# Performance work log

Hardware: AMD Instinct MI355X
Metric: run time of the kernel (lower is better)

Reference implementation:

```python
import jax, jax.numpy as jnp
import numpy as np

# ---- static configuration (mirrors EarthSpecificBlock/EarthAttention3D) ----
WS = (2, 6, 12)                 # window_size (Z, H, W)
DIM = 192
HEADS = 6
DEPTH = 2
B, Z, H, W = 1, 8, 91, 180      # token grid entering the layer
PAD_H = (WS[1] - H % WS[1]) % WS[1]   # 5
PAD_W = (WS[2] - W % WS[2]) % WS[2]   # 0
HP, WP = H + PAD_H, W + PAD_W         # 96, 180
TOK = WS[0] * WS[1] * WS[2]           # 144 tokens per window
NZ, NH, NW = Z // WS[0], HP // WS[1], WP // WS[2]   # 4, 16, 15
TYPE_W = NZ * NH                      # 64 window types (Z x lat)
BIAS_ROWS = (2 * WS[2] - 1) * WS[1] * WS[1] * WS[0] * WS[0]  # 3312


def _construct_index():
    """Position index into the earth-specific bias table (EarthAttention3D._construct_index)."""
    zi = np.arange(WS[0]); zj = -np.arange(WS[0]) * WS[0]
    hi = np.arange(WS[1]); hj = -np.arange(WS[1]) * WS[1]
    w = np.arange(WS[2])
    c1 = np.stack(np.meshgrid(zi, hi, w, indexing='ij')).reshape(3, -1)
    c2 = np.stack(np.meshgrid(zj, hj, w, indexing='ij')).reshape(3, -1)
    coords = (c1[:, :, None] - c2[:, None, :]).transpose(1, 2, 0)
    coords[:, :, 2] += WS[2] - 1
    coords[:, :, 1] *= 2 * WS[2] - 1
    coords[:, :, 0] *= (2 * WS[2] - 1) * WS[1] * WS[1]
    return coords.sum(-1).reshape(-1)   # (TOK*TOK,)


def _gen_mask():
    """Shifted-window attention mask (gen_mask), shape (1, NW, TYPE_W, 1, TOK, TOK)."""
    m = np.zeros((1, Z, HP, WP, 1), np.float32)
    zs = (slice(0, -WS[0]), slice(-WS[0], -WS[0] // 2), slice(-WS[0] // 2, None))
    hs = (slice(0, -WS[1]), slice(-WS[1], -WS[1] // 2), slice(-WS[1] // 2, None))
    cnt = 0
    for zsl in zs:
        for hsl in hs:
            m[:, zsl, hsl, :, :] = cnt
            cnt += 1
    mw = m.reshape(1, NZ, WS[0], NH, WS[1], NW, WS[2], 1).transpose(0, 1, 3, 5, 2, 4, 6, 7)
    mw = mw.reshape(1, NZ, NH, NW, TOK)
    am = mw[:, :, :, :, None, :] - mw[:, :, :, :, :, None]
    am = np.where(am != 0, np.float32(-100.0), np.float32(0.0))
    return am.transpose(0, 3, 1, 2, 4, 5).reshape(1, NW, TYPE_W, 1, TOK, TOK)


POS_IDX = jnp.asarray(_construct_index())
MASK = jnp.asarray(_gen_mask())


def _ln(x, g, b):
    m = x.mean(-1, keepdims=True)
    v = ((x - m) ** 2).mean(-1, keepdims=True)
    return (x - m) * jax.lax.rsqrt(v + 1e-5) * g + b


def _block(x, qkv_w, qkv_b, proj_w, proj_b, bias_tab, g1, b1, g2, b2, w1, bm1, w2, bm2, roll):
    shortcut = x
    x = jnp.pad(x, ((0, 0), (0, 0), (0, PAD_H), (0, PAD_W), (0, 0)))
    if roll:
        x = jnp.roll(x, (-(WS[0] // 2), -(WS[1] // 2), -(WS[2] // 2)), axis=(1, 2, 3))
    # window partition: (B, NW, TYPE_W, TOK, C)
    xw = x.reshape(B, NZ, WS[0], NH, WS[1], NW, WS[2], DIM).transpose(0, 5, 1, 3, 2, 4, 6, 7)
    xw = xw.reshape(B, NW, TYPE_W, TOK, DIM)
    dh = DIM // HEADS
    qkv = (xw @ qkv_w + qkv_b).reshape(B, NW, TYPE_W, TOK, 3, HEADS, dh)
    qkv = qkv.transpose(4, 0, 1, 2, 5, 3, 6)   # (3, B, NW, TYPE_W, HEADS, TOK, dh)
    q, k, v = qkv[0], qkv[1], qkv[2]
    q = q * (dh ** -0.5)
    attn = jnp.einsum('bwphid,bwphjd->bwphij', q, k)
    bias = bias_tab[POS_IDX].reshape(TOK, TOK, TYPE_W, HEADS).transpose(2, 3, 0, 1)
    attn = attn + bias
    if roll:
        attn = attn + MASK
    attn = jax.nn.softmax(attn, axis=-1)
    out = jnp.einsum('bwphij,bwphjd->bwphid', attn, v)
    out = out.transpose(0, 1, 2, 4, 3, 5).reshape(B, NW, TYPE_W, TOK, DIM)
    out = out @ proj_w + proj_b
    # window merge back to (B, Z, HP, WP, C)
    x = out.reshape(B, NW, NZ, NH, WS[0], WS[1], WS[2], DIM).transpose(0, 2, 4, 3, 5, 1, 6, 7)
    x = x.reshape(B, Z, HP, WP, DIM)
    if roll:
        x = jnp.roll(x, (WS[0] // 2, WS[1] // 2, WS[2] // 2), axis=(1, 2, 3))
    x = x[:, :, :H, :W]
    x = shortcut + _ln(x, g1, b1)           # post-norm residual, as in source
    h = jax.nn.gelu(x @ w1 + bm1, approximate=False)
    h = h @ w2 + bm2
    return x + _ln(h, g2, b2)


def setup_inputs() -> dict:
    key = jax.random.key(0)
    ks = jax.random.split(key, 8)
    s = 0.02
    return {
        'x': jax.random.normal(ks[0], (B, Z, H, W, DIM), jnp.float32),
        'qkv_w': jax.random.normal(ks[1], (DEPTH, DIM, 3 * DIM), jnp.float32) * s,
        'qkv_b': jnp.zeros((DEPTH, 3 * DIM), jnp.float32),
        'proj_w': jax.random.normal(ks[2], (DEPTH, DIM, DIM), jnp.float32) * s,
        'proj_b': jnp.zeros((DEPTH, DIM), jnp.float32),
        'bias_tab': jax.random.normal(ks[3], (DEPTH, BIAS_ROWS, TYPE_W, HEADS), jnp.float32) * s,
        'norm1_g': jnp.ones((DEPTH, DIM), jnp.float32),
        'norm1_b': jnp.zeros((DEPTH, DIM), jnp.float32),
        'norm2_g': jnp.ones((DEPTH, DIM), jnp.float32),
        'norm2_b': jnp.zeros((DEPTH, DIM), jnp.float32),
        'mlp_w1': jax.random.normal(ks[4], (DEPTH, DIM, 4 * DIM), jnp.float32) * s,
        'mlp_b1': jnp.zeros((DEPTH, 4 * DIM), jnp.float32),
        'mlp_w2': jax.random.normal(ks[5], (DEPTH, 4 * DIM, DIM), jnp.float32) * s,
        'mlp_b2': jnp.zeros((DEPTH, DIM), jnp.float32),
    }


def reference(x, qkv_w, qkv_b, proj_w, proj_b, bias_tab, norm1_g, norm1_b,
              norm2_g, norm2_b, mlp_w1, mlp_b1, mlp_w2, mlp_b2):
    for i in range(DEPTH):
        x = _block(x, qkv_w[i], qkv_b[i], proj_w[i], proj_b[i], bias_tab[i],
                   norm1_g[i], norm1_b[i], norm2_g[i], norm2_b[i],
                   mlp_w1[i], mlp_b1[i], mlp_w2[i], mlp_b2[i], roll=(i % 2 == 1))
    return x
```

## Files before the change

### kernel.cpp

```cpp
#include <hip/hip_runtime.h>
#include <math.h>

#define NTOK   131040
#define NTOKW  138240

typedef __attribute__((ext_vector_type(8))) short bf16x8;
typedef __attribute__((ext_vector_type(8))) unsigned short u16x8;
typedef __attribute__((ext_vector_type(4))) float f32x4;
typedef __attribute__((ext_vector_type(2))) float f32x2;

__device__ __forceinline__ float b2f(unsigned short u){
  union { unsigned u; float f; } v; v.u = ((unsigned)u) << 16; return v.f;
}
__device__ __forceinline__ unsigned short f2b(float f){
  union { float f; unsigned u; } v; v.f = f;
  unsigned r = v.u + 0x7FFFu + ((v.u >> 16) & 1u);
  return (unsigned short)(r >> 16);
}
__device__ __forceinline__ float gelu_fast(float x){
  float t = 0.79788456080286536f * (x + 0.044715f * x * x * x);
  float e = __expf(2.0f * t);
  float th = 1.0f - 2.0f * __builtin_amdgcn_rcpf(e + 1.0f);
  return 0.5f * x * (1.0f + th);
}
__device__ __forceinline__ unsigned pk_bf16(float lo, float hi){
  unsigned r;
  asm("v_cvt_pk_bf16_f32 %0, %1, %2" : "=v"(r) : "v"(lo), "v"(hi));
  return r;
}
__device__ __forceinline__ void lds_barrier(){
  asm volatile("s_waitcnt lgkmcnt(0)" ::: "memory");
  __builtin_amdgcn_sched_barrier(0);
  __builtin_amdgcn_s_barrier();
  __builtin_amdgcn_sched_barrier(0);
}

__global__ __launch_bounds__(256) void transp(const float* __restrict__ src,
                                              unsigned short* __restrict__ dst,
                                              int K, int N){
  int i = blockIdx.x*256 + threadIdx.x;
  if (i < K*N){
    int n = i / K, k = i % K;
    dst[i] = f2b(src[(size_t)k*N + n]);
  }
}

__global__ __launch_bounds__(256) void bias_pre(
    const float* __restrict__ btab,
    unsigned short* __restrict__ bw,
    int roll)
{
  int gid = blockIdx.x*256 + threadIdx.x;
  int pair = gid / 20736;
  int rem  = gid % 20736;
  int i = rem / 144, j = rem % 144;
  int tw = pair / 6, head = pair % 6;
  int ia = i/72, ib = (i%72)/12, ic = i%12;
  int ja = j/72, jb = (j%72)/12, jc = j%12;
  int idx = (ia + 2*ja)*828 + (ib + 6*jb)*23 + (ic - jc + 11);
  float v = btab[(size_t)idx*384 + tw*6 + head];
  if (roll){
    int nz = tw >> 4, nh = tw & 15;
    int zi = nz*2+ia, hi = nh*6+ib, zj = nz*2+ja, hj = nh*6+jb;
    int ri = 3*((zi<6)?0:((zi<7)?1:2)) + ((hi<90)?0:((hi<93)?1:2));
    int rj = 3*((zj<6)?0:((zj<7)?1:2)) + ((hj<90)?0:((hj<93)?1:2));
    if (ri != rj) v -= 100.0f;
  }
  bw[gid] = f2b(v);
}

__global__ __launch_bounds__(256) void gather_win(const float* __restrict__ x,
                                                  unsigned short* __restrict__ xw,
                                                  int roll){
  int gid = blockIdx.x*256 + threadIdx.x;
  int row = gid / 24;
  int dp  = gid % 24;
  int tok = row % 144;
  int wt  = row / 144;
  int tw  = wt & 63;
  int w   = wt >> 6;
  int nz = tw >> 4, nh = tw & 15;
  int wz = tok / 72; int rem = tok % 72; int wh = rem / 12; int ww = rem % 12;
  int z = nz*2 + wz, h = nh*6 + wh, wc = w*12 + ww;
  if (roll){ z = (z+1)&7; h = (h+3)%96; wc = (wc+6)%180; }
  int d0 = dp*8;
  u16x8 o;
  if (h < 91){
    const float* s = x + ((size_t)((z*91 + h)*180 + wc))*192 + d0;
    #pragma unroll
    for (int i=0;i<8;i++) o[i] = f2b(s[i]);
  } else {
    #pragma unroll
    for (int i=0;i<8;i++) o[i] = 0;
  }
  *(u16x8*)(xw + (size_t)row*192 + d0) = o;
}

__global__ __launch_bounds__(512) void gemm_k192(
    const unsigned short* __restrict__ A,
    const unsigned short* __restrict__ Bt,
    const float* __restrict__ bias,
    unsigned short* __restrict__ C,
    int N)
{
  __shared__ unsigned short Bst[192][200];
  int m0 = blockIdx.x * 128;
  int n0 = blockIdx.y * 192;
  int t = threadIdx.x;
  int lane = t & 63, w = t >> 6;
  int wm = w >> 2, wn = w & 3;
  int lg = lane >> 4, lr = lane & 15;

  #pragma unroll
  for (int i=0;i<9;i++){
    int idx = t + i*512;
    int r = idx / 24, c = (idx % 24)*8;
    *(u16x8*)&Bst[r][c] = *(const u16x8*)(Bt + (size_t)(n0 + r)*192 + c);
  }
  __syncthreads();

  const unsigned short* aRow = A + (size_t)(m0 + wm*64 + lr)*192 + lg*8;

  f32x4 acc[4][3];
  #pragma unroll
  for (int a=0;a<4;a++)
    #pragma unroll
    for (int b=0;b<3;b++) acc[a][b] = (f32x4){0.f,0.f,0.f,0.f};

  bf16x8 aP[2][6];
  #pragma unroll
  for (int ks=0; ks<6; ks++) aP[0][ks] = *(const bf16x8*)(aRow + ks*32);

  #pragma unroll
  for (int rt=0; rt<4; rt++){
    if (rt < 3){
      const unsigned short* an = aRow + (size_t)(rt+1)*16*192;
      #pragma unroll
      for (int ks=0; ks<6; ks++) aP[(rt+1)&1][ks] = *(const bf16x8*)(an + ks*32);
    }
    #pragma unroll
    for (int ks=0; ks<6; ks++){
      bf16x8 b0 = *(const bf16x8*)&Bst[wn*48 +      lr][ks*32 + lg*8];
      bf16x8 b1 = *(const bf16x8*)&Bst[wn*48 + 16 + lr][ks*32 + lg*8];
      bf16x8 b2 = *(const bf16x8*)&Bst[wn*48 + 32 + lr][ks*32 + lg*8];
      bf16x8 af = aP[rt&1][ks];
      acc[rt][0] = __builtin_amdgcn_mfma_f32_16x16x32_bf16(af, b0, acc[rt][0], 0,0,0);
      acc[rt][1] = __builtin_amdgcn_mfma_f32_16x16x32_bf16(af, b1, acc[rt][1], 0,0,0);
      acc[rt][2] = __builtin_amdgcn_mfma_f32_16x16x32_bf16(af, b2, acc[rt][2], 0,0,0);
    }
  }

  #pragma unroll
  for (int rt=0; rt<4; rt++){
    #pragma unroll
    for (int fn=0; fn<3; fn++){
      int colg = n0 + wn*48 + fn*16 + lr;
      float bv = bias[colg];
      #pragma unroll
      for (int r=0;r<4;r++){
        int rowg = m0 + wm*64 + rt*16 + lg*4 + r;
        C[(size_t)rowg*N + colg] = f2b(acc[rt][fn][r] + bv);
      }
    }
  }
}

__global__ __launch_bounds__(576) void attn_win(
    const unsigned short* __restrict__ qkv,
    const unsigned short* __restrict__ bw,
    unsigned short* __restrict__ outp)
{
  __shared__ union {
    struct { unsigned short Qs[144][32]; unsigned short Ks[144][40]; } qk;
    unsigned short Ps[144][160];
  } U;
  __shared__ unsigned short Vst[32][160];

  int b = blockIdx.x;
  int head = b % 6;
  int wt = b / 6;
  int tw = wt & 63;
  int t = threadIdx.x;
  int lane = t & 63;
  int wv = t >> 6;
  int lg = lane >> 4, lr = lane & 15;

  {
    int tok = t >> 2, c0 = (t & 3)*8;
    size_t base = ((size_t)wt*144 + tok)*576 + head*32 + c0;
    u16x8 qv = *(const u16x8*)(qkv + base);
    u16x8 kv = *(const u16x8*)(qkv + base + 192);
    u16x8 vv = *(const u16x8*)(qkv + base + 384);
    u16x8 qs;
    #pragma unroll
    for (int i=0;i<8;i++) qs[i] = f2b(b2f(qv[i]) * 0.17677669529663687f);
    *(u16x8*)&U.qk.Qs[tok][c0] = qs;
    *(u16x8*)&U.qk.Ks[tok][c0] = kv;
    #pragma unroll
    for (int i=0;i<8;i++) Vst[c0+i][tok] = vv[i];
  }
  if (t < 512) Vst[t >> 4][144 + (t & 15)] = 0;
  __syncthreads();

  float s[9][4];
  {
    bf16x8 a = *(const bf16x8*)&U.qk.Qs[wv*16 + lr][lg*8];
    #pragma unroll
    for (int ct=0; ct<9; ct++){
      bf16x8 bb = *(const bf16x8*)&U.qk.Ks[ct*16 + lr][lg*8];
      f32x4 d = {0.f,0.f,0.f,0.f};
      d = __builtin_amdgcn_mfma_f32_16x16x32_bf16(a, bb, d, 0,0,0);
      s[ct][0]=d[0]; s[ct][1]=d[1]; s[ct][2]=d[2]; s[ct][3]=d[3];
    }
  }

  {
    const unsigned short* bp = bw + (size_t)(tw*6 + head)*20736;
    int i0 = wv*16 + lg*4;
    #pragma unroll
    for (int ct=0; ct<9; ct++){
      int j = ct*16 + lr;
      #pragma unroll
      for (int r=0;r<4;r++)
        s[ct][r] += b2f(bp[(i0 + r)*144 + j]);
    }
  }

  float mx[4] = {-1e30f,-1e30f,-1e30f,-1e30f};
  #pragma unroll
  for (int ct=0; ct<9; ct++)
    #pragma unroll
    for (int r=0;r<4;r++) mx[r] = fmaxf(mx[r], s[ct][r]);
  #pragma unroll
  for (int off=1; off<16; off<<=1)
    #pragma unroll
    for (int r=0;r<4;r++) mx[r] = fmaxf(mx[r], __shfl_xor(mx[r], off));
  float sm[4] = {0.f,0.f,0.f,0.f};
  #pragma unroll
  for (int ct=0; ct<9; ct++)
    #pragma unroll
    for (int r=0;r<4;r++){ s[ct][r] = __expf(s[ct][r] - mx[r]); sm[r] += s[ct][r]; }
  #pragma unroll
  for (int off=1; off<16; off<<=1)
    #pragma unroll
    for (int r=0;r<4;r++) sm[r] += __shfl_xor(sm[r], off);
  float inv[4];
  #pragma unroll
  for (int r=0;r<4;r++) inv[r] = 1.0f / sm[r];

  lds_barrier();

  #pragma unroll
  for (int ct=0; ct<9; ct++)
    #pragma unroll
    for (int r=0;r<4;r++)
      U.Ps[wv*16 + lg*4 + r][ct*16 + lr] = f2b(s[ct][r] * inv[r]);
  #pragma unroll
  for (int r=0;r<4;r++) U.Ps[wv*16 + lg*4 + r][144 + lr] = 0;
  __syncthreads();

  #pragma unroll
  for (int ct2=0; ct2<2; ct2++){
    f32x4 o = {0.f,0.f,0.f,0.f};
    #pragma unroll
    for (int kt=0; kt<5; kt++){
      bf16x8 a  = *(const bf16x8*)&U.Ps[wv*16 + lr][kt*32 + lg*8];
      bf16x8 bb = *(const bf16x8*)&Vst[ct2*16 + lr][kt*32 + lg*8];
      o = __builtin_amdgcn_mfma_f32_16x16x32_bf16(a, bb, o, 0,0,0);
    }
    size_t rb = ((size_t)wt*144 + wv*16 + lg*4)*192 + head*32 + ct2*16 + lr;
    #pragma unroll
    for (int r=0;r<4;r++) outp[rb + (size_t)r*192] = f2b(o[r]);
  }
}

__global__ __launch_bounds__(256) void unwin_ln(
  const unsigned short* __restrict__ ywin,
  const float* __restrict__ xsrc,
  const float* __restrict__ g, const float* __restrict__ bb,
  float* __restrict__ outf, unsigned short* __restrict__ outb, int roll)
{
  int tok = blockIdx.x*4 + (threadIdx.x>>6);
  if (tok >= NTOK) return;
  int lane = threadIdx.x & 63;
  int z = tok / (91*180);
  int rem = tok % (91*180);
  int h = rem / 180, wc = rem % 180;
  int zz=z, hh=h, ww=wc;
  if (roll){ zz = (z+7)&7; hh = (h+93)%96; ww = (wc+174)%180; }
  int nz = zz>>1, wz = zz&1;
  int nh = hh/6,  wh = hh%6;
  int nw = ww/12, w2 = ww%12;
  size_t row = ((size_t)(nw*64 + nz*16 + nh))*144 + wz*72 + wh*12 + w2;
  const unsigned short* yr = ywin + row*192;
  float v[3]; float s=0.f, ss=0.f;
  #pragma unroll
  for (int i=0;i<3;i++){ v[i] = b2f(yr[lane + i*64]); s += v[i]; ss += v[i]*v[i]; }
  #pragma unroll
  for (int off=32; off>=1; off>>=1){ s += __shfl_xor(s, off); ss += __shfl_xor(ss, off); }
  float mean = s * (1.0f/192.0f);
  float var = ss * (1.0f/192.0f) - mean*mean;
  float rinv = rsqrtf(var + 1e-5f);
  size_t tb = (size_t)tok*192;
  #pragma unroll
  for (int i=0;i<3;i++){
    int d = lane + i*64;
    float o = xsrc[tb + d] + ((v[i]-mean)*rinv*g[d] + bb[d]);
    outf[tb+d] = o;
    outb[tb+d] = f2b(o);
  }
}

__global__ __launch_bounds__(512) void mlp_fused_ln(
    const unsigned short* __restrict__ A,
    const unsigned short* __restrict__ W1t,
    const float* __restrict__ bias1,
    const unsigned short* __restrict__ W2t,
    const float* __restrict__ mbias2,
    const float* __restrict__ xmid,
    const float* __restrict__ lng,
    const float* __restrict__ lnb,
    float* __restrict__ outF,
    int M)
{
  __shared__ unsigned short W1s[32][196];
  __shared__ unsigned short W2s[192][44];
  __shared__ unsigned short Hs[8][32][40];
  __shared__ float b1s[768];
  __shared__ float eps[576];
  int m0 = blockIdx.x*256;
  int t = threadIdx.x, lane = t & 63, w = t >> 6;
  int lg = lane >> 4, lr = lane & 15;

  bf16x8 afrA[6], afrB[6];
  {
    int ra = m0 + w*32 + lr, rb = ra + 16;
    if (ra < M){
      const unsigned short* ap = A + (size_t)ra*192 + lg*8;
      #pragma unroll
      for (int ks=0; ks<6; ks++) afrA[ks] = *(const bf16x8*)(ap + ks*32);
    } else {
      #pragma unroll
      for (int ks=0; ks<6; ks++)
        #pragma unroll
        for (int j=0;j<8;j++) afrA[ks][j] = 0;
    }
    if (rb < M){
      const unsigned short* ap = A + (size_t)rb*192 + lg*8;
      #pragma unroll
      for (int ks=0; ks<6; ks++) afrB[ks] = *(const bf16x8*)(ap + ks*32);
    } else {
      #pragma unroll
      for (int ks=0; ks<6; ks++)
        #pragma unroll
        for (int j=0;j<8;j++) afrB[ks][j] = 0;
    }
  }

  b1s[t] = bias1[t];
  if (t < 256) b1s[512 + t] = bias1[512 + t];
  if (t < 192){ eps[t] = mbias2[t]; eps[192 + t] = lng[t]; eps[384 + t] = lnb[t]; }

  int i1r[2], i1c[2], i2r[2], i2c[2];
  #pragma unroll
  for (int i=0;i<2;i++){
    int idx = t + i*512;
    i1r[i] = idx/24; i1c[i] = (idx%24)*8;
    i2r[i] = idx/4;  i2c[i] = (idx&3)*8;
  }
  bool g2nd = (t + 512) < 768;

  u16x8 w1r[2], w2r[2];
  w1r[0] = *(const u16x8*)(W1t + (size_t)i1r[0]*192 + i1c[0]);
  w2r[0] = *(const u16x8*)(W2t + (size_t)i2r[0]*768 + i2c[0]);
  if (g2nd){
    w1r[1] = *(const u16x8*)(W1t + (size_t)i1r[1]*192 + i1c[1]);
    w2r[1] = *(const u16x8*)(W2t + (size_t)i2r[1]*768 + i2c[1]);
  }

  f32x4 accA[12], accB[12];
  #pragma unroll
  for (int i=0;i<12;i++){ accA[i] = (f32x4){0.f,0.f,0.f,0.f}; accB[i] = (f32x4){0.f,0.f,0.f,0.f}; }

  for (int it=0; it<24; ++it){
    int hc = it*32;
    *(u16x8*)&W1s[i1r[0]][i1c[0]] = w1r[0];
    *(u16x8*)&W2s[i2r[0]][i2c[0]] = w2r[0];
    if (g2nd){
      *(u16x8*)&W1s[i1r[1]][i1c[1]] = w1r[1];
      *(u16x8*)&W2s[i2r[1]][i2c[1]] = w2r[1];
    }
    if (it < 23){
      int hc2 = hc + 32;
      w1r[0] = *(const u16x8*)(W1t + (size_t)(hc2 + i1r[0])*192 + i1c[0]);
      w2r[0] = *(const u16x8*)(W2t + (size_t)i2r[0]*768 + hc2 + i2c[0]);
      if (g2nd){
        w1r[1] = *(const u16x8*)(W1t + (size_t)(hc2 + i1r[1])*192 + i1c[1]);
        w2r[1] = *(const u16x8*)(W2t + (size_t)i2r[1]*768 + hc2 + i2c[1]);
      }
    }
    lds_barrier();

    f32x4 h0a = (f32x4){0.f,0.f,0.f,0.f}, h1a = h0a, h0b = h0a, h1b = h0a;
    #pragma unroll
    for (int ks=0; ks<6; ks++){
      bf16x8 b0  = *(const bf16x8*)&W1s[2*lr    ][ks*32 + lg*8];
      bf16x8 b1f = *(const bf16x8*)&W1s[2*lr + 1][ks*32 + lg*8];
      h0a = __builtin_amdgcn_mfma_f32_16x16x32_bf16(afrA[ks], b0,  h0a, 0,0,0);
      h1a = __builtin_amdgcn_mfma_f32_16x16x32_bf16(afrA[ks], b1f, h1a, 0,0,0);
      h0b = __builtin_amdgcn_mfma_f32_16x16x32_bf16(afrB[ks], b0,  h0b, 0,0,0);
      h1b = __builtin_amdgcn_mfma_f32_16x16x32_bf16(afrB[ks], b1f, h1b, 0,0,0);
    }
    float bb0 = b1s[hc + 2*lr];
    float bb1 = b1s[hc + 2*lr + 1];
    #pragma unroll
    for (int r=0;r<4;r++){
      *(unsigned*)&Hs[w][lg*4 + r][2*lr] =
          pk_bf16(gelu_fast(h0a[r] + bb0), gelu_fast(h1a[r] + bb1));
      *(unsigned*)&Hs[w][16 + lg*4 + r][2*lr] =
          pk_bf16(gelu_fast(h0b[r] + bb0), gelu_fast(h1b[r] + bb1));
    }
    bf16x8 paA = *(const bf16x8*)&Hs[w][lr][lg*8];
    bf16x8 paB = *(const bf16x8*)&Hs[w][16 + lr][lg*8];
    #pragma unroll
    for (int f=0; f<6; f++){
      bf16x8 c0 = *(const bf16x8*)&W2s[f*32 + 2*lr    ][lg*8];
      bf16x8 c1 = *(const bf16x8*)&W2s[f*32 + 2*lr + 1][lg*8];
      accA[2*f]   = __builtin_amdgcn_mfma_f32_16x16x32_bf16(paA, c0, accA[2*f],   0,0,0);
      accA[2*f+1] = __builtin_amdgcn_mfma_f32_16x16x32_bf16(paA, c1, accA[2*f+1], 0,0,0);
      accB[2*f]   = __builtin_amdgcn_mfma_f32_16x16x32_bf16(paB, c0, accB[2*f],   0,0,0);
      accB[2*f+1] = __builtin_amdgcn_mfma_f32_16x16x32_bf16(paB, c1, accB[2*f+1], 0,0,0);
    }
    lds_barrier();
  }

  #pragma unroll
  for (int gsel=0; gsel<2; gsel++){
    f32x4* acc = gsel ? accB : accA;
    #pragma unroll
    for (int r=0;r<4;r++){
      int row = m0 + w*32 + gsel*16 + lg*4 + r;
      float s = 0.f, ss = 0.f;
      #pragma unroll
      for (int f=0; f<6; f++){
        float v0 = acc[2*f][r]   + eps[f*32 + 2*lr];
        float v1 = acc[2*f+1][r] + eps[f*32 + 2*lr + 1];
        s += v0 + v1; ss += v0*v0 + v1*v1;
      }
      #pragma unroll
      for (int off=1; off<16; off<<=1){ s += __shfl_xor(s, off); ss += __shfl_xor(ss, off); }
      float mean = s * (1.0f/192.0f);
      float var  = ss * (1.0f/192.0f) - mean*mean;
      float rinv = rsqrtf(var + 1e-5f);
      if (row < M){
        size_t base = (size_t)row*192;
        #pragma unroll
        for (int f=0; f<6; f++){
          int c0 = f*32 + 2*lr;
          float v0 = acc[2*f][r]   + eps[c0];
          float v1 = acc[2*f+1][r] + eps[c0 + 1];
          f32x2 xm = *(const f32x2*)&xmid[base + c0];
          f32x2 o;
          o[0] = xm[0] + (v0 - mean)*rinv*eps[192 + c0]     + eps[384 + c0];
          o[1] = xm[1] + (v1 - mean)*rinv*eps[192 + c0 + 1] + eps[384 + c0 + 1];
          *(f32x2*)&outF[base + c0] = o;
        }
      }
    }
  }
}

extern "C" void kernel_launch(void* const* d_in, const int* in_sizes, int n_in,
                              void* d_out, int out_size, void* d_ws, size_t ws_size,
                              hipStream_t stream)
{
  const float* x_in    = (const float*)d_in[0];
  const float* qkvw    = (const float*)d_in[1];
  const float* qkvbias = (const float*)d_in[2];
  const float* projw   = (const float*)d_in[3];
  const float* projbias= (const float*)d_in[4];
  const float* btab    = (const float*)d_in[5];
  const float* n1g = (const float*)d_in[6];
  const float* n1b = (const float*)d_in[7];
  const float* n2g = (const float*)d_in[8];
  const float* n2b = (const float*)d_in[9];
  const float* w1  = (const float*)d_in[10];
  const float* b1  = (const float*)d_in[11];
  const float* w2  = (const float*)d_in[12];
  const float* b2  = (const float*)d_in[13];
  float* outp = (float*)d_out;

  const size_t REG_A = (size_t)NTOKW*192;
  const size_t REG_B = (size_t)NTOKW*576;
  const size_t W_QT  = (size_t)2*576*192;
  const size_t W_PT  = (size_t)2*192*192;
  const size_t W_1T  = (size_t)2*768*192;
  const size_t W_2T  = (size_t)2*192*768;
  const size_t TOT_SH = REG_A + REG_B + W_QT + W_PT + W_1T + W_2T;
  const size_t NEEDED = TOT_SH*2 + (size_t)NTOK*192*4;
  if (ws_size < NEEDED) return;

  unsigned short* ws16 = (unsigned short*)d_ws;
  size_t off = 0;
  unsigned short* regA = ws16 + off; off += REG_A;
  unsigned short* regB = ws16 + off; off += REG_B;
  unsigned short* wqt  = ws16 + off; off += W_QT;
  unsigned short* wpt  = ws16 + off; off += W_PT;
  unsigned short* w1t  = ws16 + off; off += W_1T;
  unsigned short* w2t  = ws16 + off; off += W_2T;
  float* xmidf = (float*)(ws16 + off);
  unsigned short* bw = (unsigned short*)xmidf;

  for (int dep=0; dep<2; dep++){
    transp<<<(192*576+255)/256,256,0,stream>>>(qkvw + (size_t)dep*192*576,
                                               wqt + (size_t)dep*576*192, 192, 576);
    transp<<<(192*192+255)/256,256,0,stream>>>(projw + (size_t)dep*192*192,
                                               wpt + (size_t)dep*192*192, 192, 192);
    transp<<<(192*768+255)/256,256,0,stream>>>(w1 + (size_t)dep*192*768,
                                               w1t + (size_t)dep*768*192, 192, 768);
    transp<<<(768*192+255)/256,256,0,stream>>>(w2 + (size_t)dep*768*192,
                                               w2t + (size_t)dep*192*768, 768, 192);
  }

  for (int dep=0; dep<2; dep++){
    int roll = dep;
    const float* xs = (dep==0) ? x_in : outp;
    float* xout = outp;

    gather_win<<<NTOKW*24/256, 256, 0, stream>>>(xs, regA, roll);

    dim3 g1(NTOKW/128, 3);
    gemm_k192<<<g1, 512, 0, stream>>>(regA, wqt + (size_t)dep*576*192,
                                      qkvbias + dep*576, regB, 576);

    bias_pre<<<(64*6*20736)/256, 256, 0, stream>>>(btab + (size_t)dep*3312*384, bw, roll);

    attn_win<<<960*6, 576, 0, stream>>>(regB, bw, regA);

    dim3 g2(NTOKW/128, 1);
    gemm_k192<<<g2, 512, 0, stream>>>(regA, wpt + (size_t)dep*192*192,
                                      projbias + dep*192, regB, 192);

    unwin_ln<<<NTOK/4, 256, 0, stream>>>(regB, xs, n1g + dep*192, n1b + dep*192,
                                         xmidf, regA, roll);

    mlp_fused_ln<<<(NTOK+255)/256, 512, 0, stream>>>(
        regA, w1t + (size_t)dep*768*192, b1 + dep*768,
        w2t + (size_t)dep*192*768, b2 + dep*192,
        xmidf, n2g + dep*192, n2b + dep*192, xout, NTOK);
  }
}
```

Measured before the change: 1.083 ms.

## Pre-swizzle attention bias into MFMA fragment order and shrink MLP block size

The bias precompute kernel now writes the per-window bias in the exact register-fragment order used by the attention kernel, padded to five 8-wide vectors per lane. Attention threads can then load their bias with five 16-byte vector loads issued before the barrier, instead of 36 scattered scalar bf16 loads after the QK MFMA. Separately, the fused MLP kernel moves to 256 threads and 128 rows per block, doubling the grid and changing the W1 LDS padding, which shifts occupancy and the weight-staging work per block. The padded bias layout writes slightly more data.

```diff
diff --git a/kernel.cpp b/kernel.cpp
--- a/kernel.cpp
+++ b/kernel.cpp
@@ -51,22 +51,34 @@
     int roll)
 {
   int gid = blockIdx.x*256 + threadIdx.x;
-  int pair = gid / 20736;
-  int rem  = gid % 20736;
-  int i = rem / 144, j = rem % 144;
-  int tw = pair / 6, head = pair % 6;
-  int ia = i/72, ib = (i%72)/12, ic = i%12;
-  int ja = j/72, jb = (j%72)/12, jc = j%12;
-  int idx = (ia + 2*ja)*828 + (ib + 6*jb)*23 + (ic - jc + 11);
-  float v = btab[(size_t)idx*384 + tw*6 + head];
-  if (roll){
-    int nz = tw >> 4, nh = tw & 15;
-    int zi = nz*2+ia, hi = nh*6+ib, zj = nz*2+ja, hj = nh*6+jb;
-    int ri = 3*((zi<6)?0:((zi<7)?1:2)) + ((hi<90)?0:((hi<93)?1:2));
-    int rj = 3*((zj<6)?0:((zj<7)?1:2)) + ((hj<90)?0:((hj<93)?1:2));
-    if (ri != rj) v -= 100.0f;
-  }
-  bw[gid] = f2b(v);
+  int e    = gid % 40;
+  int rem  = gid / 40;
+  int lane = rem % 64;
+  int rem2 = rem / 64;
+  int wv   = rem2 % 9;
+  int slice= rem2 / 9;
+  unsigned short out = 0;
+  if (e < 36){
+    int ct = e >> 2, r = e & 3;
+    int i = wv*16 + (lane>>4)*4 + r;
+    int j = ct*16 + (lane & 15);
+    int tw = slice / 6, head = slice % 6;
+    int ia = i/72, ib = (i%72)/12, ic = i%12;
+    int ja = j/72, jb = (j%72)/12, jc = j%12;
+    int idx = (ia + 2*ja)*828 + (ib + 6*jb)*23 + (ic - jc + 11);
+    float v = btab[(size_t)idx*384 + tw*6 + head];
+    if (roll){
+      int nz = tw >> 4, nh = tw & 15;
+      int zi = nz*2+ia, hi = nh*6+ib, zj = nz*2+ja, hj = nh*6+jb;
+      int ri = 3*((zi<6)?0:((zi<7)?1:2)) + ((hi<90)?0:((hi<93)?1:2));
+      int rj = 3*((zj<6)?0:((zj<7)?1:2)) + ((hj<90)?0:((hj<93)?1:2));
+      if (ri != rj) v -= 100.0f;
+    }
+    out = f2b(v);
+  }
+  int vec = e >> 3, elem = e & 7;
+  size_t di = ((((size_t)slice*9 + wv)*5 + vec)*64 + lane)*8 + elem;
+  bw[di] = out;
 }
 
 __global__ __launch_bounds__(256) void gather_win(const float* __restrict__ x,
@@ -200,6 +212,16 @@
     for (int i=0;i<8;i++) Vst[c0+i][tok] = vv[i];
   }
   if (t < 512) Vst[t >> 4][144 + (t & 15)] = 0;
+
+  u16x8 bv0, bv1, bv2, bv3, bv4;
+  {
+    size_t sbase = ((((size_t)(tw*6 + head))*9 + wv)*5*64 + lane)*8;
+    bv0 = *(const u16x8*)(bw + sbase);
+    bv1 = *(const u16x8*)(bw + sbase + 64*8);
+    bv2 = *(const u16x8*)(bw + sbase + 2*64*8);
+    bv3 = *(const u16x8*)(bw + sbase + 3*64*8);
+    bv4 = *(const u16x8*)(bw + sbase + 4*64*8);
+  }
   __syncthreads();
 
   float s[9][4];
@@ -214,15 +236,17 @@
     }
   }
 
-  {
-    const unsigned short* bp = bw + (size_t)(tw*6 + head)*20736;
-    int i0 = wv*16 + lg*4;
-    #pragma unroll
-    for (int ct=0; ct<9; ct++){
-      int j = ct*16 + lr;
-      #pragma unroll
-      for (int r=0;r<4;r++)
-        s[ct][r] += b2f(bp[(i0 + r)*144 + j]);
+  #pragma unroll
+  for (int ct=0; ct<9; ct++){
+    #pragma unroll
+    for (int r=0;r<4;r++){
+      const int e = ct*4 + r;
+      unsigned short bu =
+        (e < 8)  ? bv0[e & 7] :
+        (e < 16) ? bv1[e & 7] :
+        (e < 24) ? bv2[e & 7] :
+        (e < 32) ? bv3[e & 7] : bv4[e & 7];
+      s[ct][r] += b2f(bu);
     }
   }
 
@@ -311,7 +335,7 @@
   }
 }
 
-__global__ __launch_bounds__(512) void mlp_fused_ln(
+__global__ __launch_bounds__(256) void mlp_fused_ln(
     const unsigned short* __restrict__ A,
     const unsigned short* __restrict__ W1t,
     const float* __restrict__ bias1,
@@ -323,12 +347,12 @@
     float* __restrict__ outF,
     int M)
 {
-  __shared__ unsigned short W1s[32][196];
+  __shared__ unsigned short W1s[32][204];
   __shared__ unsigned short W2s[192][44];
-  __shared__ unsigned short Hs[8][32][40];
+  __shared__ unsigned short Hs[4][32][40];
   __shared__ float b1s[768];
   __shared__ float eps[576];
-  int m0 = blockIdx.x*256;
+  int m0 = blockIdx.x*128;
   int t = threadIdx.x, lane = t & 63, w = t >> 6;
   int lg = lane >> 4, lr = lane & 15;
 
@@ -358,24 +382,23 @@
   }
 
   b1s[t] = bias1[t];
-  if (t < 256) b1s[512 + t] = bias1[512 + t];
+  b1s[t + 256] = bias1[t + 256];
+  b1s[t + 512] = bias1[t + 512];
   if (t < 192){ eps[t] = mbias2[t]; eps[192 + t] = lng[t]; eps[384 + t] = lnb[t]; }
 
-  int i1r[2], i1c[2], i2r[2], i2c[2];
-  #pragma unroll
-  for (int i=0;i<2;i++){
-    int idx = t + i*512;
+  int i1r[3], i1c[3], i2r[3], i2c[3];
+  #pragma unroll
+  for (int i=0;i<3;i++){
+    int idx = t + i*256;
     i1r[i] = idx/24; i1c[i] = (idx%24)*8;
     i2r[i] = idx/4;  i2c[i] = (idx&3)*8;
   }
-  bool g2nd = (t + 512) < 768;
-
-  u16x8 w1r[2], w2r[2];
-  w1r[0] = *(const u16x8*)(W1t + (size_t)i1r[0]*192 + i1c[0]);
-  w2r[0] = *(const u16x8*)(W2t + (size_t)i2r[0]*768 + i2c[0]);
-  if (g2nd){
-    w1r[1] = *(const u16x8*)(W1t + (size_t)i1r[1]*192 + i1c[1]);
-    w2r[1] = *(const u16x8*)(W2t + (size_t)i2r[1]*768 + i2c[1]);
+
+  u16x8 w1r[3], w2r[3];
+  #pragma unroll
+  for (int i=0;i<3;i++){
+    w1r[i] = *(const u16x8*)(W1t + (size_t)i1r[i]*192 + i1c[i]);
+    w2r[i] = *(const u16x8*)(W2t + (size_t)i2r[i]*768 + i2c[i]);
   }
 
   f32x4 accA[12], accB[12];
@@ -384,19 +407,17 @@
 
   for (int it=0; it<24; ++it){
     int hc = it*32;
-    *(u16x8*)&W1s[i1r[0]][i1c[0]] = w1r[0];
-    *(u16x8*)&W2s[i2r[0]][i2c[0]] = w2r[0];
-    if (g2nd){
-      *(u16x8*)&W1s[i1r[1]][i1c[1]] = w1r[1];
-      *(u16x8*)&W2s[i2r[1]][i2c[1]] = w2r[1];
+    #pragma unroll
+    for (int i=0;i<3;i++){
+      *(u16x8*)&W1s[i1r[i]][i1c[i]] = w1r[i];
+      *(u16x8*)&W2s[i2r[i]][i2c[i]] = w2r[i];
     }
     if (it < 23){
       int hc2 = hc + 32;
-      w1r[0] = *(const u16x8*)(W1t + (size_t)(hc2 + i1r[0])*192 + i1c[0]);
-      w2r[0] = *(const u16x8*)(W2t + (size_t)i2r[0]*768 + hc2 + i2c[0]);
-      if (g2nd){
-        w1r[1] = *(const u16x8*)(W1t + (size_t)(hc2 + i1r[1])*192 + i1c[1]);
-        w2r[1] = *(const u16x8*)(W2t + (size_t)i2r[1]*768 + hc2 + i2c[1]);
+      #pragma unroll
+      for (int i=0;i<3;i++){
+        w1r[i] = *(const u16x8*)(W1t + (size_t)(hc2 + i1r[i])*192 + i1c[i]);
+        w2r[i] = *(const u16x8*)(W2t + (size_t)i2r[i]*768 + hc2 + i2c[i]);
       }
     }
     lds_barrier();
@@ -533,7 +554,7 @@
     gemm_k192<<<g1, 512, 0, stream>>>(regA, wqt + (size_t)dep*576*192,
                                       qkvbias + dep*576, regB, 576);
 
-    bias_pre<<<(64*6*20736)/256, 256, 0, stream>>>(btab + (size_t)dep*3312*384, bw, roll);
+    bias_pre<<<(384*9*64*40)/256, 256, 0, stream>>>(btab + (size_t)dep*3312*384, bw, roll);
 
     attn_win<<<960*6, 576, 0, stream>>>(regB, bw, regA);
 
@@ -544,7 +565,7 @@
     unwin_ln<<<NTOK/4, 256, 0, stream>>>(regB, xs, n1g + dep*192, n1b + dep*192,
                                          xmidf, regA, roll);
 
-    mlp_fused_ln<<<(NTOK+255)/256, 512, 0, stream>>>(
+    mlp_fused_ln<<<(NTOK+127)/128, 256, 0, stream>>>(
         regA, w1t + (size_t)dep*768*192, b1 + dep*768,
         w2t + (size_t)dep*192*768, b2 + dep*192,
         xmidf, n2g + dep*192, n2b + dep*192, xout, NTOK);
```

Measured after the change: 1.185 ms. 1.09x slower.
